# Kernel optimization log

Hardware: AMD Instinct MI355X
Metric: run time of the kernel (lower is better)

## Reference

```python
import jax, jax.numpy as jnp
import numpy as np

NUM_EMBEDDINGS = 8192
EMBEDDING_DIM = 256


def setup_inputs() -> dict:
    key = jax.random.key(0)
    k1, k2 = jax.random.split(key)
    z = jax.random.normal(k1, (16, EMBEDDING_DIM, 32, 32), dtype=jnp.float32)
    # nn.Embedding default init: N(0, 1)
    emb_table = jax.random.normal(k2, (NUM_EMBEDDINGS, EMBEDDING_DIM), dtype=jnp.float32)
    return {"z": z, "emb_table": emb_table}


def reference(z, emb_table):
    # z: [B, D, H, W]; emb_table: [K, D]
    B, D, H, W = z.shape
    # flatten to per-token vectors: [B*H*W, D]
    zf = z.reshape(B, D, H * W).transpose(0, 2, 1).reshape(B * H * W, D)
    Wt = jax.lax.stop_gradient(emb_table)  # original detaches W for distance
    # argmin of mean squared distance == argmin of squared distance;
    # expand ||z - w||^2 = ||z||^2 - 2 z.w + ||w||^2 (avoid (N,K,D) expansion)
    z_sq = jnp.sum(zf * zf, axis=-1, keepdims=True)          # [N, 1]
    w_sq = jnp.sum(Wt * Wt, axis=-1)                          # [K]
    dists = z_sq - 2.0 * (zf @ Wt.T) + w_sq                   # [N, K]
    token_ids = jnp.argmin(dists, axis=-1)                    # [N]
    quantized = emb_table[token_ids]                          # [N, D] (differentiable gather)
    return quantized.reshape(B, H * W, D).transpose(0, 2, 1).reshape(B, D, H, W)
```

## Files before the change

### kernel.cpp

```cpp
#include <hip/hip_runtime.h>
#include <stdint.h>

#define DIM 256
#define NEMB 8192
#define NTOK 16384
#define HW 1024

typedef __attribute__((ext_vector_type(4))) int int4v;

__device__ __forceinline__ void async_cp16(void* lds, const void* g) {
  __builtin_amdgcn_global_load_lds(
      (const __attribute__((address_space(1))) unsigned int*)g,
      (__attribute__((address_space(3))) unsigned int*)lds, 16, 0, 0);
}
__device__ __forceinline__ int q0_of(float x) {
  int q = __float2int_rn(x * 20.0f);
  return q > 127 ? 127 : (q < -127 ? -127 : q);
}
__device__ __forceinline__ int q1_of(float x, int q0) {
  float e = x * 20.0f - (float)q0;
  int q = __float2int_rn(e * 128.0f);
  return q > 127 ? 127 : (q < -127 ? -127 : q);
}
__device__ __forceinline__ unsigned int pack4(int a, int b, int c, int d) {
  return (unsigned int)(a & 0xff) | ((unsigned int)(b & 0xff) << 8) |
         ((unsigned int)(c & 0xff) << 16) | ((unsigned int)(d & 0xff) << 24);
}
__device__ __forceinline__ unsigned int med3u(unsigned int a, unsigned int b,
                                              unsigned int c) {
  unsigned int m;
  asm("v_med3_u32 %0, %1, %2, %3" : "=v"(m) : "v"(a), "v"(b), "v"(c));
  return m;
}
__device__ __forceinline__ void top3_insert(unsigned int v, unsigned int& m1,
                                            unsigned int& m2, unsigned int& m3) {
  unsigned int t2 = med3u(v, m1, m2);
  unsigned int t3 = med3u(v, m2, m3);
  m1 = v < m1 ? v : m1;
  m2 = t2;
  m3 = t3;
}

__global__ __launch_bounds__(256) void prep_kernel(
    const float* __restrict__ emb, unsigned int* __restrict__ q0w,
    unsigned int* __restrict__ q1w, int* __restrict__ iwsq2,
    const float* __restrict__ z, unsigned int* __restrict__ q0z) {
  __shared__ float tile[64][65];
  int tid = threadIdx.x;
  int lane = tid & 63;
  if (blockIdx.x < 2048) {
    int row = blockIdx.x * 4 + (tid >> 6);
    const float4 v = *(const float4*)(emb + (size_t)row * DIM + lane * 4);
    float s = v.x * v.x + v.y * v.y + v.z * v.z + v.w * v.w;
    int a0 = q0_of(v.x), b0 = q0_of(v.y), c0 = q0_of(v.z), d0 = q0_of(v.w);
    q0w[row * (DIM / 4) + lane] = pack4(a0, b0, c0, d0);
    q1w[row * (DIM / 4) + lane] =
        pack4(q1_of(v.x, a0), q1_of(v.y, b0), q1_of(v.z, c0), q1_of(v.w, d0));
#pragma unroll
    for (int off = 32; off > 0; off >>= 1) s += __shfl_xor(s, off, 64);
    if (lane == 0) iwsq2[row] = (int)rintf(s * 25600.0f) + 8192;
    return;
  }
  int idx = blockIdx.x - 2048;
  int b = idx >> 6, d0 = ((idx >> 4) & 3) * 64, hw0 = (idx & 15) * 64;
  int grp = tid >> 6;
  const float* src = z + (size_t)b * DIM * HW + hw0 + lane;
#pragma unroll
  for (int i = 0; i < 16; i++) {
    int dl = grp + i * 4;
    tile[dl][lane] = src[(size_t)(d0 + dl) * HW];
  }
  __syncthreads();
  int dq = tid & 15;
#pragma unroll
  for (int p = 0; p < 4; p++) {
    int n = (tid >> 4) + p * 16;
    int a0 = q0_of(tile[dq * 4 + 0][n]), b0 = q0_of(tile[dq * 4 + 1][n]);
    int c0 = q0_of(tile[dq * 4 + 2][n]), e0 = q0_of(tile[dq * 4 + 3][n]);
    int token = b * HW + hw0 + n;
    q0z[(size_t)token * (DIM / 4) + (d0 >> 2) + dq] = pack4(a0, b0, c0, e0);
  }
}

__global__ __launch_bounds__(512) void gemm_topk_kernel(
    const signed char* __restrict__ q0z, const signed char* __restrict__ q0w,
    const signed char* __restrict__ q1w, const int* __restrict__ iwsq2,
    uint4* __restrict__ partials) {
  __shared__ __align__(16) signed char sB[2][4][32 * 128];

  const int bid = blockIdx.x;
  const int kq = bid & 7;
  const int tg = bid >> 3;
  const int tid = threadIdx.x;
  const int lane = tid & 63, w = tid >> 6;
  const int c = lane & 15, quad = lane >> 4;
  const int n0 = tg * 256;
  const int k0g = kq * 1024;

  int4v af0[2][4];
#pragma unroll
  for (int t = 0; t < 2; t++) {
    const size_t arow = (size_t)(n0 + w * 32 + t * 16 + c) * DIM;
#pragma unroll
    for (int s = 0; s < 4; s++)
      af0[t][s] = *(const int4v*)(q0z + arow + s * 64 + quad * 16);
  }

  const int hi = tid >> 8;
  const int t2 = tid & 255;
  const int srow = t2 >> 3;
  const int scl = ((t2 & 7) ^ (srow & 7)) * 16;
  const signed char* p = (hi ? q1w : q0w) + (size_t)(k0g + srow) * DIM + scl;
  signed char* d0s = &sB[0][hi * 2][t2 * 16];
  signed char* d1s = &sB[0][hi * 2 + 1][t2 * 16];
  async_cp16(d0s, p);
  async_cp16(d1s, p + 128);
  p += 32 * DIM;
  __syncthreads();

  unsigned int m1[8], m2[8], m3[8];
#pragma unroll
  for (int i = 0; i < 8; i++) {
    m1[i] = 0xFFFFFFFFu; m2[i] = 0xFFFFFFFFu; m3[i] = 0xFFFFFFFFu;
  }

  unsigned int idxA = (unsigned)(k0g + c);
  const int4v zero = {0, 0, 0, 0};

  for (int it = 0; it < 32; it++) {
    const int buf = it & 1;
    if (it + 1 < 32) {
      const int nb = buf ^ 1;
      async_cp16(d0s + nb * 16384, p);
      async_cp16(d1s + nb * 16384, p + 128);
      p += 32 * DIM;
    }
    const int iw0 = iwsq2[k0g + it * 32 + c];
    const int iw1 = iwsq2[k0g + it * 32 + 16 + c];

    int4v a[2][2];
#pragma unroll
    for (int s = 0; s < 4; s++) {
      const int ph = ((((s & 1) << 2) + quad) ^ (c & 7)) * 16;
      int4v b0a = *(const int4v*)(&sB[buf][s >> 1][c * 128 + ph]);
      int4v b0b = *(const int4v*)(&sB[buf][s >> 1][(16 + c) * 128 + ph]);
      if (s == 0) {
#pragma unroll
        for (int t = 0; t < 2; t++) {
          a[t][0] = __builtin_amdgcn_mfma_i32_16x16x64_i8(af0[t][0], b0a, zero, 0, 0, 0);
          a[t][1] = __builtin_amdgcn_mfma_i32_16x16x64_i8(af0[t][0], b0b, zero, 0, 0, 0);
        }
      } else {
#pragma unroll
        for (int t = 0; t < 2; t++) {
          a[t][0] = __builtin_amdgcn_mfma_i32_16x16x64_i8(af0[t][s], b0a, a[t][0], 0, 0, 0);
          a[t][1] = __builtin_amdgcn_mfma_i32_16x16x64_i8(af0[t][s], b0b, a[t][1], 0, 0, 0);
        }
      }
    }
#pragma unroll
    for (int t = 0; t < 2; t++)
#pragma unroll
      for (int cn = 0; cn < 2; cn++)
#pragma unroll
        for (int r = 0; r < 4; r++) a[t][cn][r] <<= 7;
#pragma unroll
    for (int s = 0; s < 4; s++) {
      const int ph = ((((s & 1) << 2) + quad) ^ (c & 7)) * 16;
      int4v b1a = *(const int4v*)(&sB[buf][2 + (s >> 1)][c * 128 + ph]);
      int4v b1b = *(const int4v*)(&sB[buf][2 + (s >> 1)][(16 + c) * 128 + ph]);
#pragma unroll
      for (int t = 0; t < 2; t++) {
        a[t][0] = __builtin_amdgcn_mfma_i32_16x16x64_i8(af0[t][s], b1a, a[t][0], 0, 0, 0);
        a[t][1] = __builtin_amdgcn_mfma_i32_16x16x64_i8(af0[t][s], b1b, a[t][1], 0, 0, 0);
      }
    }
#pragma unroll
    for (int t = 0; t < 2; t++) {
#pragma unroll
      for (int r = 0; r < 4; r++) {
        unsigned int s0 = (unsigned int)(iw0 - a[t][0][r]);
        unsigned int s1 = (unsigned int)(iw1 - a[t][1][r]);
        unsigned int smin = s0 < s1 ? s0 : s1;
        unsigned int idx = s1 < s0 ? idxA + 16 : idxA;
        smin = smin < 0x1FFFFFFu ? smin : 0x1FFFFFFu;
        unsigned int pk = ((smin >> 6) << 13) | idx;
        top3_insert(pk, m1[t * 4 + r], m2[t * 4 + r], m3[t * 4 + r]);
      }
    }
    idxA += 32;
    __syncthreads();
  }

#pragma unroll
  for (int ix = 0; ix < 8; ix++) {
    unsigned int a1 = m1[ix], a2 = m2[ix], a3 = m3[ix];
#pragma unroll
    for (int off = 1; off < 16; off <<= 1) {
      unsigned int o1 = __shfl_xor(a1, off, 16);
      unsigned int o2 = __shfl_xor(a2, off, 16);
      unsigned int o3 = __shfl_xor(a3, off, 16);
      top3_insert(o1, a1, a2, a3);
      top3_insert(o2, a1, a2, a3);
      top3_insert(o3, a1, a2, a3);
    }
    m1[ix] = a1; m2[ix] = a2; m3[ix] = a3;
  }
  if (c == 0) {
#pragma unroll
    for (int t = 0; t < 2; t++) {
#pragma unroll
      for (int r = 0; r < 4; r++) {
        int token = n0 + w * 32 + t * 16 + quad * 4 + r;
        partials[(size_t)kq * NTOK + token] =
            make_uint4(m1[t * 4 + r], m2[t * 4 + r], m3[t * 4 + r], 0xFFFFFFFFu);
      }
    }
  }
}

__global__ __launch_bounds__(256) void rescore_gather_kernel(
    const uint4* __restrict__ partials, const float* __restrict__ z,
    const float* __restrict__ emb, float* __restrict__ out) {
  __shared__ float tile[32][257];
  __shared__ int sid[32];
  __shared__ int wl[32];
  __shared__ int nwl;
  const int b = blockIdx.x >> 5;
  const int hw0 = (blockIdx.x & 31) * 32;
  const int tid = threadIdx.x;
  if (tid == 0) nwl = 0;
  __syncthreads();
  {
    const int tl = tid >> 3, sub = tid & 7;
    const int token = b * HW + hw0 + tl;
    uint4 e = partials[(size_t)sub * NTOK + token];
    unsigned int m = e.x < e.y ? e.x : e.y;
    m = e.z < m ? e.z : m;
#pragma unroll
    for (int off = 1; off < 8; off <<= 1) {
      unsigned int o = __shfl_xor(m, off, 8);
      m = o < m ? o : m;
    }
    const unsigned int thr = (m >> 13) + 1536;
    int cnt = (((e.x >> 13) <= thr) ? 1 : 0) + (((e.y >> 13) <= thr) ? 1 : 0) +
              (((e.z >> 13) <= thr) ? 1 : 0);
#pragma unroll
    for (int off = 1; off < 8; off <<= 1) cnt += __shfl_xor(cnt, off, 8);
    if (sub == 0) {
      if (cnt == 1) {
        sid[tl] = (int)(m & 0x1FFFu);
      } else {
        int i = atomicAdd(&nwl, 1);
        wl[i] = tl;
      }
    }
  }
  __syncthreads();
  {
    const int w = tid >> 6, lane = tid & 63;
    for (int i = w; i < nwl; i += 4) {
      const int tl = wl[i];
      const int token = b * HW + hw0 + tl;
      unsigned int p[24];
#pragma unroll
      for (int q = 0; q < 8; q++) {
        uint4 t = partials[(size_t)q * NTOK + token];
        p[q * 3] = t.x;
        p[q * 3 + 1] = t.y;
        p[q * 3 + 2] = t.z;
      }
      unsigned int smin = p[0];
#pragma unroll
      for (int q = 1; q < 24; q++) smin = p[q] < smin ? p[q] : smin;
      const unsigned int thr = (smin >> 13) + 1536;
      float zv[4];
#pragma unroll
      for (int j = 0; j < 4; j++)
        zv[j] = z[(size_t)b * DIM * HW + (size_t)(lane * 4 + j) * HW + hw0 + tl];
      double best = 1e300;
      int bid2 = NEMB;
#pragma unroll
      for (int q = 0; q < 24; q++) {
        if ((p[q] >> 13) <= thr) {
          int id = (int)(p[q] & 0x1FFFu);
          const float4 wv = *(const float4*)(emb + (size_t)id * DIM + lane * 4);
          double s = (double)wv.x * ((double)wv.x - 2.0 * (double)zv[0]) +
                     (double)wv.y * ((double)wv.y - 2.0 * (double)zv[1]) +
                     (double)wv.z * ((double)wv.z - 2.0 * (double)zv[2]) +
                     (double)wv.w * ((double)wv.w - 2.0 * (double)zv[3]);
#pragma unroll
          for (int off = 32; off > 0; off >>= 1) s += __shfl_xor(s, off, 64);
          if (s < best || (s == best && id < bid2)) {
            best = s;
            bid2 = id;
          }
        }
      }
      if (lane == 0) sid[tl] = bid2;
    }
  }
  __syncthreads();
  for (int i = 0; i < 32; i++)
    tile[i][tid] = emb[(size_t)sid[i] * DIM + tid];
  __syncthreads();
  int h = tid & 31, dg = tid >> 5;
  for (int i = 0; i < 32; i++) {
    int d = i * 8 + dg;
    out[(size_t)b * DIM * HW + (size_t)d * HW + hw0 + h] = tile[h][d];
  }
}

extern "C" void kernel_launch(void* const* d_in, const int* in_sizes, int n_in,
                              void* d_out, int out_size, void* d_ws, size_t ws_size,
                              hipStream_t stream) {
  const float* z = (const float*)d_in[0];
  const float* emb = (const float*)d_in[1];
  float* out = (float*)d_out;
  char* ws = (char*)d_ws;

  signed char* q0w = (signed char*)(ws);
  signed char* q1w = (signed char*)(ws + 2097152);
  signed char* q0z = (signed char*)(ws + 4194304);
  int* iwsq2 = (int*)(ws + 8388608);
  uint4* partials = (uint4*)(ws + 8421376);

  prep_kernel<<<dim3(3072), 256, 0, stream>>>(
      emb, (unsigned int*)q0w, (unsigned int*)q1w, iwsq2, z, (unsigned int*)q0z);
  gemm_topk_kernel<<<dim3(512), 512, 0, stream>>>(q0z, q0w, q1w, iwsq2,
                                                  partials);
  rescore_gather_kernel<<<dim3(512), 256, 0, stream>>>(partials, z, emb, out);
}
```

Baseline: 159.7 us.

## Flatten rescore to per-candidate work items and split gather into separate kernel

The rescore stage now builds a per-block list of (token, candidate) entries and spreads them across wavefronts. Previously each wavefront rescored all candidates of one ambiguous token serially. A small serial pass then picks the best per token. The partials layout becomes token-major so each token's eight partial entries are contiguous. The gather/transpose moves into its own kernel, which adds a launch and an index round-trip through global memory, and the per-token argmin loop over the entry list is serial.

```diff
diff --git a/kernel.cpp b/kernel.cpp
--- a/kernel.cpp
+++ b/kernel.cpp
@@ -212,29 +212,29 @@
 #pragma unroll
       for (int r = 0; r < 4; r++) {
         int token = n0 + w * 32 + t * 16 + quad * 4 + r;
-        partials[(size_t)kq * NTOK + token] =
+        partials[(size_t)token * 8 + kq] =
             make_uint4(m1[t * 4 + r], m2[t * 4 + r], m3[t * 4 + r], 0xFFFFFFFFu);
       }
     }
   }
 }
 
-__global__ __launch_bounds__(256) void rescore_gather_kernel(
+__global__ __launch_bounds__(256) void rescore_kernel(
     const uint4* __restrict__ partials, const float* __restrict__ z,
-    const float* __restrict__ emb, float* __restrict__ out) {
-  __shared__ float tile[32][257];
+    const float* __restrict__ emb, int* __restrict__ sid_g) {
+  __shared__ int ent[768];
+  __shared__ double scr[768];
   __shared__ int sid[32];
-  __shared__ int wl[32];
-  __shared__ int nwl;
+  __shared__ int nent;
   const int b = blockIdx.x >> 5;
   const int hw0 = (blockIdx.x & 31) * 32;
   const int tid = threadIdx.x;
-  if (tid == 0) nwl = 0;
+  if (tid == 0) nent = 0;
   __syncthreads();
   {
     const int tl = tid >> 3, sub = tid & 7;
     const int token = b * HW + hw0 + tl;
-    uint4 e = partials[(size_t)sub * NTOK + token];
+    uint4 e = partials[(size_t)token * 8 + sub];
     unsigned int m = e.x < e.y ? e.x : e.y;
     m = e.z < m ? e.z : m;
 #pragma unroll
@@ -243,63 +243,75 @@
       m = o < m ? o : m;
     }
     const unsigned int thr = (m >> 13) + 1536;
-    int cnt = (((e.x >> 13) <= thr) ? 1 : 0) + (((e.y >> 13) <= thr) ? 1 : 0) +
-              (((e.z >> 13) <= thr) ? 1 : 0);
+    const int c0 = ((e.x >> 13) <= thr) ? 1 : 0;
+    const int c1 = ((e.y >> 13) <= thr) ? 1 : 0;
+    const int c2 = ((e.z >> 13) <= thr) ? 1 : 0;
+    int cnt = c0 + c1 + c2;
 #pragma unroll
     for (int off = 1; off < 8; off <<= 1) cnt += __shfl_xor(cnt, off, 8);
-    if (sub == 0) {
-      if (cnt == 1) {
-        sid[tl] = (int)(m & 0x1FFFu);
-      } else {
-        int i = atomicAdd(&nwl, 1);
-        wl[i] = tl;
-      }
-    }
-  }
-  __syncthreads();
+    if (cnt == 1) {
+      if (sub == 0) sid[tl] = (int)(m & 0x1FFFu);
+    } else {
+      const int k = c0 + c1 + c2;
+      if (k) {
+        int j = atomicAdd(&nent, k);
+        if (c0) ent[j++] = (tl << 16) | (int)(e.x & 0x1FFFu);
+        if (c1) ent[j++] = (tl << 16) | (int)(e.y & 0x1FFFu);
+        if (c2) ent[j] = (tl << 16) | (int)(e.z & 0x1FFFu);
+      }
+      if (sub == 0) sid[tl] = -1;
+    }
+  }
+  __syncthreads();
+  const int ne = nent;
   {
     const int w = tid >> 6, lane = tid & 63;
-    for (int i = w; i < nwl; i += 4) {
-      const int tl = wl[i];
-      const int token = b * HW + hw0 + tl;
-      unsigned int p[24];
-#pragma unroll
-      for (int q = 0; q < 8; q++) {
-        uint4 t = partials[(size_t)q * NTOK + token];
-        p[q * 3] = t.x;
-        p[q * 3 + 1] = t.y;
-        p[q * 3 + 2] = t.z;
-      }
-      unsigned int smin = p[0];
-#pragma unroll
-      for (int q = 1; q < 24; q++) smin = p[q] < smin ? p[q] : smin;
-      const unsigned int thr = (smin >> 13) + 1536;
+    for (int i = w; i < ne; i += 4) {
+      const int en = ent[i];
+      const int tl = en >> 16, id = en & 0x1FFF;
       float zv[4];
 #pragma unroll
       for (int j = 0; j < 4; j++)
         zv[j] = z[(size_t)b * DIM * HW + (size_t)(lane * 4 + j) * HW + hw0 + tl];
-      double best = 1e300;
-      int bid2 = NEMB;
-#pragma unroll
-      for (int q = 0; q < 24; q++) {
-        if ((p[q] >> 13) <= thr) {
-          int id = (int)(p[q] & 0x1FFFu);
-          const float4 wv = *(const float4*)(emb + (size_t)id * DIM + lane * 4);
-          double s = (double)wv.x * ((double)wv.x - 2.0 * (double)zv[0]) +
-                     (double)wv.y * ((double)wv.y - 2.0 * (double)zv[1]) +
-                     (double)wv.z * ((double)wv.z - 2.0 * (double)zv[2]) +
-                     (double)wv.w * ((double)wv.w - 2.0 * (double)zv[3]);
-#pragma unroll
-          for (int off = 32; off > 0; off >>= 1) s += __shfl_xor(s, off, 64);
-          if (s < best || (s == best && id < bid2)) {
-            best = s;
-            bid2 = id;
-          }
+      const float4 wv = *(const float4*)(emb + (size_t)id * DIM + lane * 4);
+      double s = (double)wv.x * ((double)wv.x - 2.0 * (double)zv[0]) +
+                 (double)wv.y * ((double)wv.y - 2.0 * (double)zv[1]) +
+                 (double)wv.z * ((double)wv.z - 2.0 * (double)zv[2]) +
+                 (double)wv.w * ((double)wv.w - 2.0 * (double)zv[3]);
+#pragma unroll
+      for (int off = 32; off > 0; off >>= 1) s += __shfl_xor(s, off, 64);
+      if (lane == 0) scr[i] = s;
+    }
+  }
+  __syncthreads();
+  if (tid < 32 && sid[tid] < 0) {
+    double best = 1e300;
+    int bid2 = NEMB;
+    for (int i = 0; i < ne; i++) {
+      if ((ent[i] >> 16) == tid) {
+        const double s = scr[i];
+        const int id = ent[i] & 0x1FFF;
+        if (s < best || (s == best && id < bid2)) {
+          best = s;
+          bid2 = id;
         }
       }
-      if (lane == 0) sid[tl] = bid2;
-    }
-  }
+    }
+    sid[tid] = bid2;
+  }
+  __syncthreads();
+  if (tid < 32) sid_g[b * HW + hw0 + tid] = sid[tid];
+}
+
+__global__ __launch_bounds__(256) void gather_kernel(
+    const int* __restrict__ sid_g, const float* __restrict__ emb,
+    float* __restrict__ out) {
+  __shared__ float tile[32][257];
+  __shared__ int sid[32];
+  const int b = blockIdx.x >> 5;
+  const int hw0 = (blockIdx.x & 31) * 32;
+  const int tid = threadIdx.x;
+  if (tid < 32) sid[tid] = sid_g[b * HW + hw0 + tid];
   __syncthreads();
   for (int i = 0; i < 32; i++)
     tile[i][tid] = emb[(size_t)sid[i] * DIM + tid];
@@ -324,10 +336,12 @@
   signed char* q0z = (signed char*)(ws + 4194304);
   int* iwsq2 = (int*)(ws + 8388608);
   uint4* partials = (uint4*)(ws + 8421376);
+  int* sid_g = (int*)(ws + 10518528);
 
   prep_kernel<<<dim3(3072), 256, 0, stream>>>(
       emb, (unsigned int*)q0w, (unsigned int*)q1w, iwsq2, z, (unsigned int*)q0z);
   gemm_topk_kernel<<<dim3(512), 512, 0, stream>>>(q0z, q0w, q1w, iwsq2,
                                                   partials);
-  rescore_gather_kernel<<<dim3(512), 256, 0, stream>>>(partials, z, emb, out);
-}
+  rescore_kernel<<<dim3(512), 256, 0, stream>>>(partials, z, emb, sid_g);
+  gather_kernel<<<dim3(512), 256, 0, stream>>>(sid_g, emb, out);
+}
```

Measured after the change: 170.5 us. 6.8% more time.
